# Kernel tuning notes

Measured on AMD Instinct MI355X. Metric: run time of the kernel, lower is better.

The kernel has to match this reference:

```python
import jax, jax.numpy as jnp
import numpy as np

T_NO = 100
COS_BASIS_NO = 19
COS_SHIFT = 1.0
COS_SCALE = 5.0
SUB_NO = 10
T_DATA = 50000
E_NO = 2000
I_NO = 500


def make_cos_basis():
    # [cos_basis_no, T_no] raised-cosine log-time basis, matching the torch loop
    x = jnp.arange(T_NO, dtype=jnp.float32)
    raw = COS_SCALE * jnp.log(x + COS_SHIFT)                       # [T_no]
    phi = (jnp.pi / 2.0) * jnp.arange(COS_BASIS_NO, dtype=jnp.float32)[:, None]  # [B,1]
    basis = 0.5 * jnp.cos(raw[None, :] - phi) + 0.5
    mask = (raw[None, :] >= phi - jnp.pi) & (raw[None, :] <= phi + jnp.pi)
    return jnp.where(mask, basis, 0.0)


def causal_filter(sig, kern):
    # sig [T, sub], kern [sub, T_no] (un-flipped); causal conv: out[t]=sum_tau kern[:,tau]*sig[t-tau]
    sub, t_no = kern.shape
    pad = jnp.concatenate([jnp.zeros((t_no - 1, sub), sig.dtype), sig], axis=0)  # left-pad
    lhs = pad.T[None]                      # [1, sub, T+T_no-1]
    rhs = kern[:, ::-1][:, None, :]        # flipped kernel [sub, 1, T_no]
    out = jax.lax.conv_general_dilated(lhs, rhs, window_strides=(1,), padding='VALID',
                                       feature_group_count=sub)
    return out[0].T                        # [T, sub]


def setup_inputs() -> dict:
    key = jax.random.key(0)
    ks = jax.random.split(key, 10)
    # sparse binary spike trains
    S_e = (jax.random.uniform(ks[0], (T_DATA, E_NO)) < 0.02).astype(jnp.float32)
    S_i = (jax.random.uniform(ks[1], (T_DATA, I_NO)) < 0.02).astype(jnp.float32)
    # binary-tree dendrite connectivity: C_den[parent, child]=1, child index > parent
    C = np.zeros((SUB_NO, SUB_NO), np.float32)
    for p in range(SUB_NO):
        for c in (2 * p + 1, 2 * p + 2):
            if c < SUB_NO:
                C[p, c] = 1.0
    C_den = jnp.asarray(C)
    # one-hot synapse->subunit assignment
    ae = jax.random.randint(ks[2], (E_NO,), 0, SUB_NO)
    ai = jax.random.randint(ks[3], (I_NO,), 0, SUB_NO)
    C_syn_e = jax.nn.one_hot(ae, SUB_NO, dtype=jnp.float32).T   # [sub, E]
    C_syn_i = jax.nn.one_hot(ai, SUB_NO, dtype=jnp.float32).T   # [sub, I]
    W_syn = 0.1 * jax.random.normal(ks[4], (SUB_NO, COS_BASIS_NO, 2), jnp.float32)
    W_hist = 0.05 * jax.random.normal(ks[5], (SUB_NO, COS_BASIS_NO), jnp.float32)
    W_sub = 0.5 * jnp.ones((SUB_NO,), jnp.float32)
    V_o = jax.random.normal(ks[6], (1,), jnp.float32)
    Theta = 0.05 * jax.random.normal(ks[7], (SUB_NO,), jnp.float32)
    return dict(S_e=S_e, S_i=S_i, C_den=C_den, C_syn_e=C_syn_e, C_syn_i=C_syn_i,
                W_syn=W_syn, W_hist=W_hist, W_sub=W_sub, V_o=V_o, Theta=Theta)


def reference(S_e, S_i, C_den, C_syn_e, C_syn_i, W_syn, W_hist, W_sub, V_o, Theta):
    cos_basis = make_cos_basis()                          # [B, T_no]
    e_kern = W_syn[:, :, 0] @ cos_basis                   # [sub, T_no]
    i_kern = W_syn[:, :, 1] @ cos_basis
    hist_kern = W_hist @ cos_basis                        # [sub, T_no]
    # spike_convolve
    syn_e = S_e @ C_syn_e.T                               # [T, sub]
    syn_i = S_i @ C_syn_i.T
    syn = causal_filter(syn_e, e_kern) + causal_filter(syn_i, i_kern)  # [T, sub]
    # test_forward sequential scan with a [T_no, sub] ring buffer of past ns_out
    hist_kern_f = hist_kern[:, ::-1]                      # flipped, as in torch test_forward
    W2 = W_sub ** 2

    def step(buf, syn_t):
        # buf[k] == ns_out[t+k]; buf[0] is ns_out[t] (oldest)
        hist = jnp.einsum('ks,sk->s', buf, hist_kern_f)   # windowed history filter
        prop = (buf[0] * W2) @ C_den.T                    # tree propagation
        new = jnp.tanh(syn_t + hist + prop + Theta)
        buf = jnp.concatenate([buf[1:], new[None]], axis=0)
        return buf, new

    buf0 = jnp.zeros((T_NO, SUB_NO), syn.dtype)
    _, ns_out = jax.lax.scan(step, buf0, syn)             # ns_out [T, sub]
    final_V = ns_out[:, 0] * W2[0] + V_o[0]               # [T]
    out_filters = jnp.concatenate([e_kern, i_kern, hist_kern], axis=0)  # [3*sub, T_no]
    return final_V, out_filters
```

## Files before the change

kernel.cpp:

```cpp
#include <hip/hip_runtime.h>
#include <hip/hip_fp16.h>

#define T_DATA 50000
#define E_NO 2000
#define I_NO 500
#define NS 10
#define NB 19
#define NT 100
#define T_PADR 50176
#define KSC 2.8853900817779268f

#define OFF_H     0
#define OFF_EK    5120
#define OFF_IK    10240
#define OFF_WP    15360
#define OFF_AE    15488
#define OFF_AI    17536
#define OFF_FLAGS 18048
#define OFF_PRE   18112
#define WS_NEED   1021632u

__device__ __forceinline__ float loadF(const void* p, long i, int dt) {
    if (dt == 0) return ((const float*)p)[i];
    if (dt == 1) {
        unsigned v = (unsigned)((const unsigned short*)p)[i] << 16;
        return __uint_as_float(v);
    }
    return __half2float(((const __half*)p)[i]);
}

__global__ void probe_kernel(const unsigned* cand0, const unsigned* cand1,
                             int* flags)
{
    unsigned a = cand0[0], b = cand1[0];
    int ca = -1, cb = -1;
    if (a == 0x3F000000u) ca = 0; else if (a == 0x3F003F00u) ca = 1;
    else if (a == 0x38003800u) ca = 2;
    if (b == 0x3F000000u) cb = 0; else if (b == 0x3F003F00u) cb = 1;
    else if (b == 0x38003800u) cb = 2;
    int dt, sw;
    if (ca >= 0)      { dt = ca; sw = 0; }
    else if (cb >= 0) { dt = cb; sw = 1; }
    else              { dt = 0;  sw = 0; }
    flags[0] = dt; flags[1] = sw;
}

__global__ __launch_bounds__(256) void prep_kernel(
    const void* __restrict__ W_syn,
    const void* __restrict__ W_hist,
    const void* __restrict__ ws_c0,
    const void* __restrict__ ws_c1,
    const void* __restrict__ C_den,
    const void* __restrict__ C_syn_e,
    const void* __restrict__ C_syn_i,
    const int* __restrict__ flags,
    unsigned char* __restrict__ ws,
    float* __restrict__ out_filters)
{
    const int dt = flags[0];
    const void* W_sub = flags[1] ? ws_c1 : ws_c0;
    float* h_s  = (float*)(ws + OFF_H);
    float* ek   = (float*)(ws + OFF_EK);
    float* ik   = (float*)(ws + OFF_IK);
    float* wp   = (float*)(ws + OFF_WP);
    unsigned char* ae = ws + OFF_AE;
    unsigned char* ai = ws + OFF_AI;
    const int tid = threadIdx.x;
    const float PI  = 3.14159265358979323846f;
    const float HPI = 1.57079632679489662f;

    for (int idx = tid; idx < 3000; idx += 256) {
        int row = idx / 100, x = idx % 100;
        int typ = row / 10, s = row % 10;
        float raw = 5.0f * logf((float)x + 1.0f);
        float acc = 0.0f;
        for (int b = 0; b < NB; ++b) {
            float phi = HPI * (float)b;
            float d = raw - phi;
            if (d >= -PI && d <= PI) {
                float w;
                if (typ == 0)      w = loadF(W_syn, (long)(s*NB + b)*2 + 0, dt);
                else if (typ == 1) w = loadF(W_syn, (long)(s*NB + b)*2 + 1, dt);
                else               w = loadF(W_hist, (long)(s*NB + b), dt);
                acc = fmaf(w, 0.5f * cosf(d) + 0.5f, acc);
            }
        }
        out_filters[row*100 + x] = acc;
        if (typ == 0)      ek[s*128 + x] = acc;
        else if (typ == 1) ik[s*128 + x] = acc;
        else               h_s[s*128 + x] = acc * KSC;
    }
    for (int e = tid; e < E_NO; e += 256) {
        unsigned char a = 0;
        for (int s = 0; s < NS; ++s)
            if (loadF(C_syn_e, (long)s*E_NO + e, dt) > 0.5f) a = (unsigned char)s;
        ae[e] = a;
    }
    for (int e = tid; e < I_NO; e += 256) {
        unsigned char a = 0;
        for (int s = 0; s < NS; ++s)
            if (loadF(C_syn_i, (long)s*I_NO + e, dt) > 0.5f) a = (unsigned char)s;
        ai[e] = a;
    }
    if (tid < NS) {
        int s = tid;
        int c1 = 2*s + 1, c2 = 2*s + 2;
        float v1 = 0.f, v2 = 0.f;
        if (c1 < NS) { float w = loadF(W_sub, c1, dt); v1 = KSC * loadF(C_den, s*NS + c1, dt) * w * w; }
        if (c2 < NS) { float w = loadF(W_sub, c2, dt); v2 = KSC * loadF(C_den, s*NS + c2, dt) * w * w; }
        wp[2*s] = v1; wp[2*s + 1] = v2;
    }
}

__global__ __launch_bounds__(256) void convf_kernel(
    const void* __restrict__ S_e,
    const void* __restrict__ S_i,
    const unsigned char* __restrict__ ae,
    const unsigned char* __restrict__ ai,
    const float* __restrict__ ek,
    const float* __restrict__ ik,
    const void* __restrict__ th_c0,
    const void* __restrict__ th_c1,
    const int* __restrict__ flags,
    __half* __restrict__ pre)
{
    __shared__ float se[355][11];
    __shared__ float si[355][11];
    __shared__ float k_e[NS][NT];
    __shared__ float k_i[NS][NT];
    const int dt = flags[0];
    const void* Theta = flags[1] ? th_c0 : th_c1;
    const int tid = threadIdx.x;
    const int T0 = blockIdx.x * 256;

    for (int idx = tid; idx < NS*NT; idx += 256) {
        int s = idx / NT, u = idx % NT;
        k_e[s][u] = ek[s*128 + u];
        k_i[s][u] = ik[s*128 + u];
    }
    for (int idx = tid; idx < 355*11; idx += 256) {
        (&se[0][0])[idx] = 0.f;
        (&si[0][0])[idx] = 0.f;
    }
    __syncthreads();

    const bool interior = (T0 >= 99) && (T0 + 256 <= T_DATA);
    if (dt == 0) {
        if (interior) {
            const uint4* baseE = (const uint4*)((const float*)S_e + (size_t)(T0-99)*E_NO);
            for (int w = tid; w < 355*500; w += 256) {
                uint4 v = baseE[w];
                if (v.x | v.y | v.z | v.w) {
                    int rr = w / 500, e0 = (w - rr*500) * 4;
                    if (v.x) atomicAdd(&se[rr][ae[e0 + 0]], 1.0f);
                    if (v.y) atomicAdd(&se[rr][ae[e0 + 1]], 1.0f);
                    if (v.z) atomicAdd(&se[rr][ae[e0 + 2]], 1.0f);
                    if (v.w) atomicAdd(&se[rr][ae[e0 + 3]], 1.0f);
                }
            }
            const uint4* baseI = (const uint4*)((const float*)S_i + (size_t)(T0-99)*I_NO);
            for (int w = tid; w < 355*125; w += 256) {
                uint4 v = baseI[w];
                if (v.x | v.y | v.z | v.w) {
                    int rr = w / 125, e0 = (w - rr*125) * 4;
                    if (v.x) atomicAdd(&si[rr][ai[e0 + 0]], 1.0f);
                    if (v.y) atomicAdd(&si[rr][ai[e0 + 1]], 1.0f);
                    if (v.z) atomicAdd(&si[rr][ai[e0 + 2]], 1.0f);
                    if (v.w) atomicAdd(&si[rr][ai[e0 + 3]], 1.0f);
                }
            }
        } else {
            for (int w = tid; w < 355*500; w += 256) {
                int rr = w / 500, c = w - rr*500;
                int t = T0 - 99 + rr;
                if (t < 0 || t >= T_DATA) continue;
                uint4 v = ((const uint4*)((const float*)S_e + (size_t)t * E_NO))[c];
                if (v.x | v.y | v.z | v.w) {
                    int e0 = c * 4;
                    if (v.x) atomicAdd(&se[rr][ae[e0 + 0]], 1.0f);
                    if (v.y) atomicAdd(&se[rr][ae[e0 + 1]], 1.0f);
                    if (v.z) atomicAdd(&se[rr][ae[e0 + 2]], 1.0f);
                    if (v.w) atomicAdd(&se[rr][ae[e0 + 3]], 1.0f);
                }
            }
            for (int w = tid; w < 355*125; w += 256) {
                int rr = w / 125, c = w - rr*125;
                int t = T0 - 99 + rr;
                if (t < 0 || t >= T_DATA) continue;
                uint4 v = ((const uint4*)((const float*)S_i + (size_t)t * I_NO))[c];
                if (v.x | v.y | v.z | v.w) {
                    int e0 = c * 4;
                    if (v.x) atomicAdd(&si[rr][ai[e0 + 0]], 1.0f);
                    if (v.y) atomicAdd(&si[rr][ai[e0 + 1]], 1.0f);
                    if (v.z) atomicAdd(&si[rr][ai[e0 + 2]], 1.0f);
                    if (v.w) atomicAdd(&si[rr][ai[e0 + 3]], 1.0f);
                }
            }
        }
    } else {
        for (int w = tid; w < 355*250; w += 256) {
            int rr = w / 250, c = w - rr*250;
            int t = T0 - 99 + rr;
            if (t < 0 || t >= T_DATA) continue;
            uint4 v = ((const uint4*)((const unsigned short*)S_e + (size_t)t * E_NO))[c];
            if (v.x | v.y | v.z | v.w) {
                int e0 = c * 8;
                #pragma unroll
                for (int q = 0; q < 4; ++q) {
                    unsigned wv = (&v.x)[q];
                    if (wv & 0xffffu) atomicAdd(&se[rr][ae[e0 + 2*q]], 1.0f);
                    if (wv >> 16)     atomicAdd(&se[rr][ae[e0 + 2*q + 1]], 1.0f);
                }
            }
        }
        for (int w = tid; w < 355*125; w += 256) {
            int rr = w / 125, c = w - rr*125;
            int t = T0 - 99 + rr;
            if (t < 0 || t >= T_DATA) continue;
            uint2 v = ((const uint2*)((const unsigned short*)S_i + (size_t)t * I_NO))[c];
            if (v.x | v.y) {
                int e0 = c * 4;
                if (v.x & 0xffffu) atomicAdd(&si[rr][ai[e0 + 0]], 1.0f);
                if (v.x >> 16)     atomicAdd(&si[rr][ai[e0 + 1]], 1.0f);
                if (v.y & 0xffffu) atomicAdd(&si[rr][ai[e0 + 2]], 1.0f);
                if (v.y >> 16)     atomicAdd(&si[rr][ai[e0 + 3]], 1.0f);
            }
        }
    }
    __syncthreads();
    const int t = T0 + tid;
    if (t >= T_PADR) return;
    if (t >= T_DATA) {
        for (int s = 0; s < NS; ++s) pre[(size_t)t*NS + s] = __float2half(0.0f);
        return;
    }
    const int lt = tid + 99;
    float accs[NS];
    #pragma unroll
    for (int s = 0; s < NS; ++s) accs[s] = 0.f;
    for (int u = 0; u < NT; ++u) {
        #pragma unroll
        for (int s = 0; s < NS; ++s)
            accs[s] += k_e[s][u]*se[lt - u][s] + k_i[s][u]*si[lt - u][s];
    }
    #pragma unroll
    for (int s = 0; s < NS; ++s)
        pre[(size_t)t*NS + s] = __float2half(KSC * (accs[s] + loadF(Theta, s, dt)));
}

__global__ __launch_bounds__(64) void scan_kernel(
    const __half* __restrict__ pre,
    const float* __restrict__ h_s,
    const float* __restrict__ wp,
    const void* __restrict__ ws_c0,
    const void* __restrict__ ws_c1,
    const void* __restrict__ V_o,
    const int* __restrict__ flags,
    float* __restrict__ outV)
{
    const int dt = flags[0];
    const void* W_sub = flags[1] ? ws_c1 : ws_c0;
    const int lane = threadIdx.x & 63;
    const int s = lane % NS;
    const int g = lane / NS;
    const bool active = (g < 6);
    const bool loader = (g == 5);
    const bool chain  = (g == 0);

    float hreg[17];
    #pragma unroll
    for (int m = 0; m < 17; ++m) {
        int j = 17*g + 2 + m;
        hreg[m] = (active && j < NT) ? h_s[s*128 + j] : 0.f;
    }
    const int jtr = 17*g + 19;
    const float htr = (active && jtr < NT) ? h_s[s*128 + jtr] : 0.f;
    const float h0r = h_s[s*128 + 0];
    const float h1r = h_s[s*128 + 1];

    float pend[17];
    #pragma unroll
    for (int k = 0; k < 17; ++k) {
        int l = (k + 1) % 17;
        int T = 17*g + l - 1;
        pend[k] = (active && T >= 0) ? __half2float(pre[(size_t)T*NS + s]) : 0.f;
    }
    float ld[17];
    #pragma unroll
    for (int j = 0; j < 17; ++j) {
        int T0 = (j == 16) ? 101 : (102 + j);
        ld[j] = __half2float(pre[(size_t)T0*NS + s]);
    }
    float upA = __shfl_down(pend[16], 10);
    float upB = __shfl_down(pend[0], 10);

    const float wl1 = loader ? wp[2*s] : 0.f;
    const float wl2 = loader ? wp[2*s + 1] : 0.f;
    const int cc1 = (2*s + 1 < NS) ? (2*s + 1) : 0;
    const int cc2 = (2*s + 2 < NS) ? (2*s + 2) : 0;
    const float Vo  = loadF(V_o, 0, dt);
    const float w0  = loadF(W_sub, 0, dt);
    const float W20 = w0 * w0;

    float nsv = 0.f, n1 = 0.f;
    float vdA = 0.f, vdB = 0.f, vdC = 0.f;
    float vc1A = 0.f, vc1B = 0.f;
    float vc2A = 0.f, vc2B = 0.f;

    for (int tb = 0; tb < T_DATA; tb += 17) {
        const __half* pb = pre + (size_t)(tb + 118)*NS + s;
        #pragma unroll
        for (int p = 0; p < 17; ++p) {
            const int t = tb + p;
            const int kw = (p + 16) % 17;
            pend[kw] = loader ? ld[kw] : upA;
            pend[kw] = fmaf(vdC, htr, pend[kw]);
            ld[kw] = __half2float(pb[p*NS]);
            #pragma unroll
            for (int m = 0; m < 17; ++m) {
                const int k2 = (p + m) % 17;
                pend[k2] = fmaf(vdA, hreg[m], pend[k2]);
            }
            {
                const int kp = (p + 12) % 17;
                pend[kp] = fmaf(wl1, vc1A, pend[kp]);
                pend[kp] = fmaf(wl2, vc2A, pend[kp]);
            }
            float upN = __shfl_down(pend[(p + 1) % 17], 10);
            float vN   = __shfl(nsv, s);
            float vc1N = __shfl(nsv, cc1);
            float vc2N = __shfl(nsv, cc2);
            float x = fmaf(nsv, h0r, fmaf(n1, h1r, pend[p]));
            float e2 = __builtin_amdgcn_exp2f(x);
            float r  = __builtin_amdgcn_rcpf(e2 + 1.0f);
            float nv = fmaf(-2.0f, r, 1.0f);
            float vout = fmaf(nv, W20, Vo);
            if (lane == 0 && t < T_DATA) outV[t] = vout;
            n1 = nsv; nsv = nv;
            vdC = vdA; vdA = vdB; vdB = vN;
            vc1A = vc1B; vc1B = vc1N;
            vc2A = vc2B; vc2B = vc2N;
            upA = upB; upB = upN;
        }
    }
}

__global__ __launch_bounds__(256) void zero_out_kernel(float* out) {
    int i = blockIdx.x * 256 + threadIdx.x;
    if (i < T_DATA + 3000) out[i] = 0.0f;
}

extern "C" void kernel_launch(void* const* d_in, const int* in_sizes, int n_in,
                              void* d_out, int out_size, void* d_ws, size_t ws_size,
                              hipStream_t stream)
{
    unsigned char* ws = (unsigned char*)d_ws;
    float* out = (float*)d_out;

    static const long EXP[10] = {100000000L, 25000000L, 100, 20000, 5000,
                                 380, 190, 10, 1, 10};
    int idx[10];
    bool ok = (n_in == 10);
    if (ok) {
        bool direct = true;
        for (int k = 0; k < 10; ++k)
            if ((long)in_sizes[k] != EXP[k]) { direct = false; break; }
        if (direct) {
            for (int k = 0; k < 10; ++k) idx[k] = k;
        } else {
            bool used[10] = {false,false,false,false,false,false,false,false,false,false};
            for (int k = 0; k < 10 && ok; ++k) {
                idx[k] = -1;
                for (int j = 0; j < 10; ++j)
                    if (!used[j] && (long)in_sizes[j] == EXP[k]) {
                        idx[k] = j; used[j] = true; break;
                    }
                if (idx[k] < 0) ok = false;
            }
        }
    }
    if (!ok || ws_size < (size_t)WS_NEED) {
        zero_out_kernel<<<208, 256, 0, stream>>>(out);
        return;
    }
    const void* S_e     = d_in[idx[0]];
    const void* S_i     = d_in[idx[1]];
    const void* C_den   = d_in[idx[2]];
    const void* C_syn_e = d_in[idx[3]];
    const void* C_syn_i = d_in[idx[4]];
    const void* W_syn   = d_in[idx[5]];
    const void* Whist   = d_in[idx[6]];
    const void* Wsub0   = d_in[idx[7]];
    const void* V_o     = d_in[idx[8]];
    const void* Wsub1   = d_in[idx[9]];
    int* flags = (int*)(ws + OFF_FLAGS);

    probe_kernel<<<1, 1, 0, stream>>>((const unsigned*)Wsub0,
                                      (const unsigned*)Wsub1, flags);
    prep_kernel<<<1, 256, 0, stream>>>(W_syn, Whist, Wsub0, Wsub1,
                                       C_den, C_syn_e, C_syn_i, flags, ws,
                                       out + T_DATA);
    convf_kernel<<<196, 256, 0, stream>>>(
        S_e, S_i, ws + OFF_AE, ws + OFF_AI,
        (const float*)(ws + OFF_EK), (const float*)(ws + OFF_IK),
        Wsub0, Wsub1, flags, (__half*)(ws + OFF_PRE));
    scan_kernel<<<1, 64, 0, stream>>>(
        (const __half*)(ws + OFF_PRE),
        (const float*)(ws + OFF_H),
        (const float*)(ws + OFF_WP),
        Wsub0, Wsub1, V_o, flags, out);
}
```

Measured before the change: 5.932 ms.

## Move tree propagation to LDS ring buffer and shorten tanh dependency chain

The scan kernel no longer carries child-subunit values through per-step cross-lane shuffles. Each step writes the new output into a shared-memory ring buffer, and the propagation term for the next block of 17 steps is read back from it in advance, removing two shuffles from the serial recurrence. The recurrence is also rewritten in terms of the reciprocal value R, with h0 and h1 folded into constants, to shorten the critical path through the tanh. The separate probe kernel is merged into prep_kernel, saving one launch. This adds LDS write/read ordering within a single wavefront and relies on the ring offset lining up with the propagation delay.

```diff
diff --git a/kernel.cpp b/kernel.cpp
--- a/kernel.cpp
+++ b/kernel.cpp
@@ -29,22 +29,6 @@
     return __half2float(((const __half*)p)[i]);
 }
 
-__global__ void probe_kernel(const unsigned* cand0, const unsigned* cand1,
-                             int* flags)
-{
-    unsigned a = cand0[0], b = cand1[0];
-    int ca = -1, cb = -1;
-    if (a == 0x3F000000u) ca = 0; else if (a == 0x3F003F00u) ca = 1;
-    else if (a == 0x38003800u) ca = 2;
-    if (b == 0x3F000000u) cb = 0; else if (b == 0x3F003F00u) cb = 1;
-    else if (b == 0x38003800u) cb = 2;
-    int dt, sw;
-    if (ca >= 0)      { dt = ca; sw = 0; }
-    else if (cb >= 0) { dt = cb; sw = 1; }
-    else              { dt = 0;  sw = 0; }
-    flags[0] = dt; flags[1] = sw;
-}
-
 __global__ __launch_bounds__(256) void prep_kernel(
     const void* __restrict__ W_syn,
     const void* __restrict__ W_hist,
@@ -53,12 +37,30 @@
     const void* __restrict__ C_den,
     const void* __restrict__ C_syn_e,
     const void* __restrict__ C_syn_i,
-    const int* __restrict__ flags,
     unsigned char* __restrict__ ws,
     float* __restrict__ out_filters)
 {
-    const int dt = flags[0];
-    const void* W_sub = flags[1] ? ws_c1 : ws_c0;
+    __shared__ int sflags[2];
+    if (threadIdx.x == 0) {
+        unsigned a = ((const unsigned*)ws_c0)[0];
+        unsigned b = ((const unsigned*)ws_c1)[0];
+        int ca = -1, cb = -1;
+        if (a == 0x3F000000u) ca = 0; else if (a == 0x3F003F00u) ca = 1;
+        else if (a == 0x38003800u) ca = 2;
+        if (b == 0x3F000000u) cb = 0; else if (b == 0x3F003F00u) cb = 1;
+        else if (b == 0x38003800u) cb = 2;
+        int dt, sw;
+        if (ca >= 0)      { dt = ca; sw = 0; }
+        else if (cb >= 0) { dt = cb; sw = 1; }
+        else              { dt = 0;  sw = 0; }
+        sflags[0] = dt; sflags[1] = sw;
+        ((int*)(ws + OFF_FLAGS))[0] = dt;
+        ((int*)(ws + OFF_FLAGS))[1] = sw;
+    }
+    __syncthreads();
+    const int dt = sflags[0];
+    const void* W_sub = sflags[1] ? ws_c1 : ws_c0;
+
     float* h_s  = (float*)(ws + OFF_H);
     float* ek   = (float*)(ws + OFF_EK);
     float* ik   = (float*)(ws + OFF_IK);
@@ -258,6 +260,7 @@
     const int* __restrict__ flags,
     float* __restrict__ outV)
 {
+    __shared__ float ring[128][NS];
     const int dt = flags[0];
     const void* W_sub = flags[1] ? ws_c1 : ws_c0;
     const int lane = threadIdx.x & 63;
@@ -267,6 +270,9 @@
     const bool loader = (g == 5);
     const bool chain  = (g == 0);
 
+    for (int i = lane; i < 128*NS; i += 64) (&ring[0][0])[i] = 0.f;
+    __syncthreads();
+
     float hreg[17];
     #pragma unroll
     for (int m = 0; m < 17; ++m) {
@@ -277,6 +283,9 @@
     const float htr = (active && jtr < NT) ? h_s[s*128 + jtr] : 0.f;
     const float h0r = h_s[s*128 + 0];
     const float h1r = h_s[s*128 + 1];
+    const float h01 = h0r + h1r;
+    const float m0n = -2.0f * h0r;
+    const float m1n = -2.0f * h1r;
 
     float pend[17];
     #pragma unroll
@@ -294,18 +303,21 @@
     float upA = __shfl_down(pend[16], 10);
     float upB = __shfl_down(pend[0], 10);
 
-    const float wl1 = loader ? wp[2*s] : 0.f;
-    const float wl2 = loader ? wp[2*s + 1] : 0.f;
+    const float w1  = wp[2*s];
+    const float w2v = wp[2*s + 1];
     const int cc1 = (2*s + 1 < NS) ? (2*s + 1) : 0;
     const int cc2 = (2*s + 2 < NS) ? (2*s + 2) : 0;
     const float Vo  = loadF(V_o, 0, dt);
     const float w0  = loadF(W_sub, 0, dt);
     const float W20 = w0 * w0;
 
-    float nsv = 0.f, n1 = 0.f;
+    float R0 = 0.5f, R1 = 0.5f;
+    float nsv = 0.f;
     float vdA = 0.f, vdB = 0.f, vdC = 0.f;
-    float vc1A = 0.f, vc1B = 0.f;
-    float vc2A = 0.f, vc2B = 0.f;
+
+    float propv[17], propn[17];
+    #pragma unroll
+    for (int q = 0; q < 17; ++q) propv[q] = 0.f;
 
     for (int tb = 0; tb < T_DATA; tb += 17) {
         const __half* pb = pre + (size_t)(tb + 118)*NS + s;
@@ -321,27 +333,26 @@
                 const int k2 = (p + m) % 17;
                 pend[k2] = fmaf(vdA, hreg[m], pend[k2]);
             }
+            float upN = __shfl_down(pend[(p + 1) % 17], 10);
+            float vN  = __shfl(nsv, s);
             {
-                const int kp = (p + 12) % 17;
-                pend[kp] = fmaf(wl1, vc1A, pend[kp]);
-                pend[kp] = fmaf(wl2, vc2A, pend[kp]);
-            }
-            float upN = __shfl_down(pend[(p + 1) % 17], 10);
-            float vN   = __shfl(nsv, s);
-            float vc1N = __shfl(nsv, cc1);
-            float vc2N = __shfl(nsv, cc2);
-            float x = fmaf(nsv, h0r, fmaf(n1, h1r, pend[p]));
+                const int rr = (t + 45) & 127;
+                propn[p] = fmaf(w1, ring[rr][cc1], w2v * ring[rr][cc2]);
+            }
+            float A  = fmaf(m1n, R1, (pend[p] + propv[p]) + h01);
+            float x  = fmaf(m0n, R0, A);
             float e2 = __builtin_amdgcn_exp2f(x);
-            float r  = __builtin_amdgcn_rcpf(e2 + 1.0f);
-            float nv = fmaf(-2.0f, r, 1.0f);
-            float vout = fmaf(nv, W20, Vo);
-            if (lane == 0 && t < T_DATA) outV[t] = vout;
-            n1 = nsv; nsv = nv;
+            float Rn = __builtin_amdgcn_rcpf(e2 + 1.0f);
+            float nv = fmaf(-2.0f, Rn, 1.0f);
+            if (chain) ring[t & 127][s] = nv;
+            if (lane == 0 && t < T_DATA) outV[t] = fmaf(nv, W20, Vo);
+            R1 = R0; R0 = Rn;
+            nsv = nv;
             vdC = vdA; vdA = vdB; vdB = vN;
-            vc1A = vc1B; vc1B = vc1N;
-            vc2A = vc2B; vc2B = vc2N;
             upA = upB; upB = upN;
         }
+        #pragma unroll
+        for (int q = 0; q < 17; ++q) propv[q] = propn[q];
     }
 }
 
@@ -395,10 +406,8 @@
     const void* Wsub1   = d_in[idx[9]];
     int* flags = (int*)(ws + OFF_FLAGS);
 
-    probe_kernel<<<1, 1, 0, stream>>>((const unsigned*)Wsub0,
-                                      (const unsigned*)Wsub1, flags);
     prep_kernel<<<1, 256, 0, stream>>>(W_syn, Whist, Wsub0, Wsub1,
-                                       C_den, C_syn_e, C_syn_i, flags, ws,
+                                       C_den, C_syn_e, C_syn_i, ws,
                                        out + T_DATA);
     convf_kernel<<<196, 256, 0, stream>>>(
         S_e, S_i, ws + OFF_AE, ws + OFF_AI,
```

Result: slower. 7.235 ms (+22.0%).
